# Performance work log

Hardware: AMD Instinct MI355X
Metric: run time of the kernel (lower is better)

The kernel has to match this reference:

```python
import jax, jax.numpy as jnp
import numpy as np

N_VERT = 100000
N_EDGE = 50000
NNZ = 3200000
IN_CH = 256
OUT_CH = 64


def setup_inputs() -> dict:
    key = jax.random.key(0)
    k1, k2, k3, k4, k5, k6 = jax.random.split(key, 6)
    X = jax.random.normal(k1, (N_VERT, IN_CH), dtype=jnp.float32)
    W = jax.random.normal(k2, (OUT_CH, IN_CH), dtype=jnp.float32) * (IN_CH ** -0.5)
    degE = jax.random.uniform(k3, (N_EDGE,), dtype=jnp.float32, minval=0.01, maxval=1.0)
    degV = jax.random.uniform(k4, (N_VERT,), dtype=jnp.float32, minval=0.01, maxval=1.0)
    Wdiag = jnp.ones((N_EDGE,), dtype=jnp.float32)
    v_idx = jax.random.randint(k5, (NNZ,), 0, N_VERT, dtype=jnp.int32)
    e_idx = jax.random.randint(k6, (NNZ,), 0, N_EDGE, dtype=jnp.int32)
    return {"X": X, "W": W, "degE": degE, "degV": degV, "Wdiag": Wdiag,
            "v_idx": v_idx, "e_idx": e_idx}


def reference(X, W, degE, degV, Wdiag, v_idx, e_idx):
    # Dense projection: [N, in] @ [in, out] -> [N, out]
    Xp = jnp.einsum('ni,oi->no', X, W)
    # Stage 1: vertex -> hyperedge aggregation, degE + Wdiag normalization
    Xe = jax.ops.segment_sum(Xp[v_idx], e_idx, num_segments=N_EDGE)
    Xe = Xe * (degE * Wdiag)[:, None]
    # Stage 2: hyperedge -> vertex aggregation, degV normalization
    Xv = jax.ops.segment_sum(Xe[e_idx], v_idx, num_segments=N_VERT)
    Xv = Xv * degV[:, None]
    return Xv
```

## Files before the change

### kernel.cpp

```cpp
#include <hip/hip_runtime.h>

#define NV   100000
#define NE   50000
#define NNZ  3200000
#define KIN  256
#define KOUT 64

#define NB    256
#define CHUNK (NNZ / NB)
#define TS    6250
#define NBE   782
#define NBV   1563
#define NBINS (NBE + NBV)
#define LSCAN (NBINS * NB)
#define NBLK_SCAN ((LSCAN + 1023) / 1024)

#define ECAP_E 6144
#define ECAP_V 4096

typedef short short8 __attribute__((ext_vector_type(8)));
typedef float f32x4  __attribute__((ext_vector_type(4)));

__device__ __forceinline__ unsigned short f2bf(float f) {
    union { float f; unsigned u; } c{f};
    const unsigned lsb = (c.u >> 16) & 1u;
    return (unsigned short)((c.u + 0x7FFFu + lsb) >> 16);
}
__device__ __forceinline__ float bf2f_lo(unsigned u) {
    union { unsigned u; float f; } c{u << 16};
    return c.f;
}
__device__ __forceinline__ float bf2f_hi(unsigned u) {
    union { unsigned u; float f; } c{u & 0xFFFF0000u};
    return c.f;
}
__device__ __forceinline__ short8 pack8(const float4 lo, const float4 hi) {
    short8 r;
    r[0] = (short)f2bf(lo.x); r[1] = (short)f2bf(lo.y);
    r[2] = (short)f2bf(lo.z); r[3] = (short)f2bf(lo.w);
    r[4] = (short)f2bf(hi.x); r[5] = (short)f2bf(hi.y);
    r[6] = (short)f2bf(hi.z); r[7] = (short)f2bf(hi.w);
    return r;
}

__global__ __launch_bounds__(256) void k_wb(const float* __restrict__ W,
                                            unsigned short* __restrict__ Wb) {
    const int i = blockIdx.x * 256 + threadIdx.x;
    Wb[i] = f2bf(W[i]);
}

__global__ __launch_bounds__(256) void k_project(const float* __restrict__ X,
                                                 const unsigned short* __restrict__ Wb,
                                                 unsigned short* __restrict__ Xpb) {
    const int tid  = threadIdx.x;
    const int lane = tid & 63;
    const int wv   = tid >> 6;
    const int l15  = lane & 15;
    const int l4   = lane >> 4;
    const int rbase = blockIdx.x * 128 + wv * 32;

    const int r0 = min(rbase + l15,      NV - 1);
    const int r1 = min(rbase + 16 + l15, NV - 1);
    const float* xp0 = X + (size_t)r0 * KIN + l4 * 8;
    const float* xp1 = X + (size_t)r1 * KIN + l4 * 8;
    const unsigned short* wp = Wb + (size_t)l15 * KIN + l4 * 8;

    f32x4 acc[2][4];
#pragma unroll
    for (int t = 0; t < 2; ++t)
#pragma unroll
        for (int g = 0; g < 4; ++g)
            acc[t][g] = (f32x4){0.f, 0.f, 0.f, 0.f};

#pragma unroll
    for (int s = 0; s < 8; ++s) {
        const int k0 = s * 32;
        const float4 a0lo = *(const float4*)(xp0 + k0);
        const float4 a0hi = *(const float4*)(xp0 + k0 + 4);
        const float4 a1lo = *(const float4*)(xp1 + k0);
        const float4 a1hi = *(const float4*)(xp1 + k0 + 4);
        short8 b[4];
#pragma unroll
        for (int g = 0; g < 4; ++g)
            b[g] = *(const short8*)(wp + (size_t)g * 16 * KIN + k0);
        const short8 a0 = pack8(a0lo, a0hi);
        const short8 a1 = pack8(a1lo, a1hi);
#pragma unroll
        for (int g = 0; g < 4; ++g) {
            acc[0][g] = __builtin_amdgcn_mfma_f32_16x16x32_bf16(a0, b[g], acc[0][g], 0, 0, 0);
            acc[1][g] = __builtin_amdgcn_mfma_f32_16x16x32_bf16(a1, b[g], acc[1][g], 0, 0, 0);
        }
    }

#pragma unroll
    for (int t = 0; t < 2; ++t)
#pragma unroll
        for (int i = 0; i < 4; ++i) {
            const int r = rbase + t * 16 + l4 * 4 + i;
            if (r < NV) {
#pragma unroll
                for (int g = 0; g < 4; ++g)
                    Xpb[(size_t)r * KOUT + g * 16 + l15] = f2bf(acc[t][g][i]);
            }
        }
}

__global__ __launch_bounds__(1024) void k_hist(const int* __restrict__ v_idx,
                                               const int* __restrict__ e_idx,
                                               int* __restrict__ mat) {
    __shared__ int h[NBINS];
    const int b = blockIdx.x, tid = threadIdx.x;
    for (int i = tid; i < NBINS; i += 1024) h[i] = 0;
    __syncthreads();
    const int base = b * CHUNK;
    for (int i = tid; i < CHUNK; i += 1024) {
        atomicAdd(&h[e_idx[base + i] >> 6], 1);
        atomicAdd(&h[NBE + (v_idx[base + i] >> 6)], 1);
    }
    __syncthreads();
    for (int j = tid; j < NBINS; j += 1024) mat[j * NB + b] = h[j];
}

__global__ __launch_bounds__(1024) void k_scan1(int* __restrict__ mat,
                                                int* __restrict__ bsum) {
    __shared__ int buf[1024];
    const int tid = threadIdx.x;
    const int i = blockIdx.x * 1024 + tid;
    const int v = (i < LSCAN) ? mat[i] : 0;
    buf[tid] = v;
    __syncthreads();
    for (int d = 1; d < 1024; d <<= 1) {
        int t = (tid >= d) ? buf[tid - d] : 0;
        __syncthreads();
        buf[tid] += t;
        __syncthreads();
    }
    if (i < LSCAN) mat[i] = buf[tid] - v;
    if (tid == 1023) bsum[blockIdx.x] = buf[1023];
}

__global__ __launch_bounds__(1024) void k_scan2(int* __restrict__ bsum) {
    __shared__ int buf[1024];
    const int tid = threadIdx.x;
    const int v = (tid < NBLK_SCAN) ? bsum[tid] : 0;
    buf[tid] = v;
    __syncthreads();
    for (int d = 1; d < 1024; d <<= 1) {
        int t = (tid >= d) ? buf[tid - d] : 0;
        __syncthreads();
        buf[tid] += t;
        __syncthreads();
    }
    if (tid < NBLK_SCAN) bsum[tid] = buf[tid] - v;
}

__global__ __launch_bounds__(1024) void k_scan3(int* __restrict__ mat,
                                                const int* __restrict__ bsum) {
    const int i = blockIdx.x * 1024 + threadIdx.x;
    if (i < LSCAN) mat[i] += bsum[blockIdx.x];
}

template <int SIDE, int NBIN>
__global__ __launch_bounds__(1024) void k_partsort(const int* __restrict__ v_idx,
                                                   const int* __restrict__ e_idx,
                                                   const int* __restrict__ mat,
                                                   unsigned* __restrict__ part) {
    __shared__ unsigned sbuf[TS];
    __shared__ unsigned short binbuf[TS];
    __shared__ int hist[NBIN], pfx[NBIN], cur[NBIN], gdst[NBIN];
    const int b = blockIdx.x, tid = threadIdx.x;
    const int rowOff = SIDE ? NBE : 0;
    const int sub    = SIDE ? NNZ : 0;

    for (int j = tid; j < NBIN; j += 1024)
        gdst[j] = mat[(rowOff + j) * NB + b] - sub;

    const int base = b * CHUNK;
    for (int tile = 0; tile < CHUNK / TS; ++tile) {
        __syncthreads();
        for (int j = tid; j < NBIN; j += 1024) hist[j] = 0;
        __syncthreads();

        int sb[7]; unsigned svv[7];
#pragma unroll
        for (int s = 0; s < 7; ++s) {
            const int li = s * 1024 + tid;
            sb[s] = -1;
            if (li < TS) {
                const int i = base + tile * TS + li;
                const int v = v_idx[i], e = e_idx[i];
                int bin; unsigned val;
                if (SIDE == 0) { bin = e >> 6; val = (unsigned)v | ((unsigned)(e & 63) << 17); }
                else           { bin = v >> 6; val = (unsigned)e | ((unsigned)(v & 63) << 17); }
                atomicAdd(&hist[bin], 1);
                sb[s] = bin; svv[s] = val;
            }
        }
        __syncthreads();

        if (tid < 64) {
            int carry = 0;
            for (int c = 0; c < NBIN; c += 64) {
                const int j = c + tid;
                const int h = (j < NBIN) ? hist[j] : 0;
                int x = h;
#pragma unroll
                for (int d = 1; d < 64; d <<= 1) {
                    const int y = __shfl_up(x, d, 64);
                    if (tid >= d) x += y;
                }
                if (j < NBIN) pfx[j] = carry + x - h;
                carry += __shfl(x, 63, 64);
            }
        }
        __syncthreads();
        for (int j = tid; j < NBIN; j += 1024) cur[j] = pfx[j];
        __syncthreads();

#pragma unroll
        for (int s = 0; s < 7; ++s) {
            if (sb[s] >= 0) {
                const int p = atomicAdd(&cur[sb[s]], 1);
                sbuf[p] = svv[s];
                binbuf[p] = (unsigned short)sb[s];
            }
        }
        __syncthreads();

        for (int li = tid; li < TS; li += 1024) {
            const int bin = binbuf[li];
            part[gdst[bin] + (li - pfx[bin])] = sbuf[li];
        }
        __syncthreads();
        for (int j = tid; j < NBIN; j += 1024) gdst[j] += cur[j] - pfx[j];
    }
}

__global__ __launch_bounds__(1024) void k_sortgatherE(const unsigned* __restrict__ part,
                                                      const int* __restrict__ mat,
                                                      const unsigned short* __restrict__ Xpb,
                                                      const float* __restrict__ degE,
                                                      const float* __restrict__ Wdiag,
                                                      unsigned short* __restrict__ Xeb) {
    __shared__ unsigned sbuf[ECAP_E];
    __shared__ int hist[64], cur[64], pfx[65];
    const int b = blockIdx.x, tid = threadIdx.x;
    const int base = mat[b * NB];
    const int end  = (b == NBE - 1) ? NNZ : mat[(b + 1) * NB];
    const int nb = end - base;

    if (tid < 64) hist[tid] = 0;
    __syncthreads();
    for (int i = tid; i < nb; i += 1024)
        atomicAdd(&hist[(part[base + i] >> 17) & 63], 1);
    __syncthreads();
    if (tid == 0) {
        int s = 0;
        for (int k = 0; k < 64; ++k) { pfx[k] = s; cur[k] = s; s += hist[k]; }
        pfx[64] = s;
    }
    __syncthreads();
    for (int i = tid; i < nb; i += 1024) {
        const unsigned u = part[base + i];
        const int p = atomicAdd(&cur[(u >> 17) & 63], 1);
        sbuf[p] = u & 0x1FFFFu;
    }
    __syncthreads();

    const int wv = tid >> 6, lane = tid & 63;
    const int q = lane >> 3, sl = lane & 7;
#pragma unroll
    for (int j = 0; j < 4; ++j) {
        const int le = wv * 4 + j;
        const int e_id = (b << 6) + le;
        const int s0 = pfx[le];
        const int n  = pfx[le + 1] - s0;
        float a0 = 0.f, a1 = 0.f, a2 = 0.f, a3 = 0.f,
              a4 = 0.f, a5 = 0.f, a6 = 0.f, a7 = 0.f;
        const int nf = n >> 3;
        int t = 0;
        for (; t + 4 <= nf; t += 4) {
            int idx[4]; uint4 u4[4];
#pragma unroll
            for (int z = 0; z < 4; ++z) idx[z] = (int)sbuf[s0 + 8 * (t + z) + q];
#pragma unroll
            for (int z = 0; z < 4; ++z)
                u4[z] = *(const uint4*)&Xpb[(size_t)idx[z] * KOUT + 8 * sl];
#pragma unroll
            for (int z = 0; z < 4; ++z) {
                a0 += bf2f_lo(u4[z].x); a1 += bf2f_hi(u4[z].x);
                a2 += bf2f_lo(u4[z].y); a3 += bf2f_hi(u4[z].y);
                a4 += bf2f_lo(u4[z].z); a5 += bf2f_hi(u4[z].z);
                a6 += bf2f_lo(u4[z].w); a7 += bf2f_hi(u4[z].w);
            }
        }
        for (; t < nf; ++t) {
            const int idx = (int)sbuf[s0 + 8 * t + q];
            const uint4 u = *(const uint4*)&Xpb[(size_t)idx * KOUT + 8 * sl];
            a0 += bf2f_lo(u.x); a1 += bf2f_hi(u.x);
            a2 += bf2f_lo(u.y); a3 += bf2f_hi(u.y);
            a4 += bf2f_lo(u.z); a5 += bf2f_hi(u.z);
            a6 += bf2f_lo(u.w); a7 += bf2f_hi(u.w);
        }
        if (n & 7) {
            const int src = nf * 8 + q;
            if (src < n) {
                const int idx = (int)sbuf[s0 + src];
                const uint4 u = *(const uint4*)&Xpb[(size_t)idx * KOUT + 8 * sl];
                a0 += bf2f_lo(u.x); a1 += bf2f_hi(u.x);
                a2 += bf2f_lo(u.y); a3 += bf2f_hi(u.y);
                a4 += bf2f_lo(u.z); a5 += bf2f_hi(u.z);
                a6 += bf2f_lo(u.w); a7 += bf2f_hi(u.w);
            }
        }
#pragma unroll
        for (int d = 8; d < 64; d <<= 1) {
            a0 += __shfl_xor(a0, d, 64); a1 += __shfl_xor(a1, d, 64);
            a2 += __shfl_xor(a2, d, 64); a3 += __shfl_xor(a3, d, 64);
            a4 += __shfl_xor(a4, d, 64); a5 += __shfl_xor(a5, d, 64);
            a6 += __shfl_xor(a6, d, 64); a7 += __shfl_xor(a7, d, 64);
        }
        if (q == 0 && e_id < NE) {
            const float s = degE[e_id] * Wdiag[e_id];
            uint4 pk;
            pk.x = (unsigned)f2bf(a0 * s) | ((unsigned)f2bf(a1 * s) << 16);
            pk.y = (unsigned)f2bf(a2 * s) | ((unsigned)f2bf(a3 * s) << 16);
            pk.z = (unsigned)f2bf(a4 * s) | ((unsigned)f2bf(a5 * s) << 16);
            pk.w = (unsigned)f2bf(a6 * s) | ((unsigned)f2bf(a7 * s) << 16);
            *(uint4*)&Xeb[(size_t)e_id * KOUT + 8 * sl] = pk;
        }
    }
}

__global__ __launch_bounds__(1024) void k_sortgatherV(const unsigned* __restrict__ part,
                                                      const int* __restrict__ mat,
                                                      const unsigned short* __restrict__ Xeb,
                                                      const float* __restrict__ degV,
                                                      float* __restrict__ out) {
    __shared__ unsigned sbuf[ECAP_V];
    __shared__ int hist[64], cur[64], pfx[65];
    const int b = blockIdx.x, tid = threadIdx.x;
    const int base = mat[NBE * NB + b * NB] - NNZ;
    const int end  = (b == NBV - 1) ? NNZ : (mat[NBE * NB + (b + 1) * NB] - NNZ);
    const int nb = end - base;

    if (tid < 64) hist[tid] = 0;
    __syncthreads();
    for (int i = tid; i < nb; i += 1024)
        atomicAdd(&hist[(part[base + i] >> 17) & 63], 1);
    __syncthreads();
    if (tid == 0) {
        int s = 0;
        for (int k = 0; k < 64; ++k) { pfx[k] = s; cur[k] = s; s += hist[k]; }
        pfx[64] = s;
    }
    __syncthreads();
    for (int i = tid; i < nb; i += 1024) {
        const unsigned u = part[base + i];
        const int p = atomicAdd(&cur[(u >> 17) & 63], 1);
        sbuf[p] = u & 0x1FFFFu;
    }
    __syncthreads();

    const int wv = tid >> 6, lane = tid & 63;
    const int q = lane >> 3, sl = lane & 7;
#pragma unroll
    for (int j = 0; j < 4; ++j) {
        const int lv = wv * 4 + j;
        const int v_id = (b << 6) + lv;
        const int s0 = pfx[lv];
        const int n  = pfx[lv + 1] - s0;
        float a0 = 0.f, a1 = 0.f, a2 = 0.f, a3 = 0.f,
              a4 = 0.f, a5 = 0.f, a6 = 0.f, a7 = 0.f;
        const int nf = n >> 3;
        int t = 0;
        for (; t + 4 <= nf; t += 4) {
            int idx[4]; uint4 u4[4];
#pragma unroll
            for (int z = 0; z < 4; ++z) idx[z] = (int)sbuf[s0 + 8 * (t + z) + q];
#pragma unroll
            for (int z = 0; z < 4; ++z)
                u4[z] = *(const uint4*)&Xeb[(size_t)idx[z] * KOUT + 8 * sl];
#pragma unroll
            for (int z = 0; z < 4; ++z) {
                a0 += bf2f_lo(u4[z].x); a1 += bf2f_hi(u4[z].x);
                a2 += bf2f_lo(u4[z].y); a3 += bf2f_hi(u4[z].y);
                a4 += bf2f_lo(u4[z].z); a5 += bf2f_hi(u4[z].z);
                a6 += bf2f_lo(u4[z].w); a7 += bf2f_hi(u4[z].w);
            }
        }
        for (; t < nf; ++t) {
            const int idx = (int)sbuf[s0 + 8 * t + q];
            const uint4 u = *(const uint4*)&Xeb[(size_t)idx * KOUT + 8 * sl];
            a0 += bf2f_lo(u.x); a1 += bf2f_hi(u.x);
            a2 += bf2f_lo(u.y); a3 += bf2f_hi(u.y);
            a4 += bf2f_lo(u.z); a5 += bf2f_hi(u.z);
            a6 += bf2f_lo(u.w); a7 += bf2f_hi(u.w);
        }
        if (n & 7) {
            const int src = nf * 8 + q;
            if (src < n) {
                const int idx = (int)sbuf[s0 + src];
                const uint4 u = *(const uint4*)&Xeb[(size_t)idx * KOUT + 8 * sl];
                a0 += bf2f_lo(u.x); a1 += bf2f_hi(u.x);
                a2 += bf2f_lo(u.y); a3 += bf2f_hi(u.y);
                a4 += bf2f_lo(u.z); a5 += bf2f_hi(u.z);
                a6 += bf2f_lo(u.w); a7 += bf2f_hi(u.w);
            }
        }
#pragma unroll
        for (int d = 8; d < 64; d <<= 1) {
            a0 += __shfl_xor(a0, d, 64); a1 += __shfl_xor(a1, d, 64);
            a2 += __shfl_xor(a2, d, 64); a3 += __shfl_xor(a3, d, 64);
            a4 += __shfl_xor(a4, d, 64); a5 += __shfl_xor(a5, d, 64);
            a6 += __shfl_xor(a6, d, 64); a7 += __shfl_xor(a7, d, 64);
        }
        if (q == 0 && v_id < NV) {
            const float s = degV[v_id];
            *(float4*)&out[(size_t)v_id * KOUT + 8 * sl] =
                make_float4(a0 * s, a1 * s, a2 * s, a3 * s);
            *(float4*)&out[(size_t)v_id * KOUT + 8 * sl + 4] =
                make_float4(a4 * s, a5 * s, a6 * s, a7 * s);
        }
    }
}

extern "C" void kernel_launch(void* const* d_in, const int* in_sizes, int n_in,
                              void* d_out, int out_size, void* d_ws, size_t ws_size,
                              hipStream_t stream) {
    const float* X     = (const float*)d_in[0];
    const float* W     = (const float*)d_in[1];
    const float* degE  = (const float*)d_in[2];
    const float* degV  = (const float*)d_in[3];
    const float* Wdiag = (const float*)d_in[4];
    const int*   v_idx = (const int*)d_in[5];
    const int*   e_idx = (const int*)d_in[6];
    float* out = (float*)d_out;

    unsigned short* Xpb  = (unsigned short*)d_ws;
    unsigned short* Xeb  = Xpb + (size_t)NV * KOUT;
    unsigned*       partE = (unsigned*)(Xeb + (size_t)NE * KOUT);
    unsigned*       partV = partE + NNZ;
    int*            mat   = (int*)(partV + NNZ);
    int*            bsum  = mat + LSCAN;
    unsigned short* Wb    = (unsigned short*)(bsum + ((NBLK_SCAN + 3) & ~3));

    k_wb<<<(KIN * KOUT) / 256, 256, 0, stream>>>(W, Wb);
    k_project<<<(NV + 127) / 128, 256, 0, stream>>>(X, Wb, Xpb);

    k_hist<<<NB, 1024, 0, stream>>>(v_idx, e_idx, mat);
    k_scan1<<<NBLK_SCAN, 1024, 0, stream>>>(mat, bsum);
    k_scan2<<<1, 1024, 0, stream>>>(bsum);
    k_scan3<<<NBLK_SCAN, 1024, 0, stream>>>(mat, bsum);

    k_partsort<0, NBE><<<NB, 1024, 0, stream>>>(v_idx, e_idx, mat, partE);
    k_partsort<1, NBV><<<NB, 1024, 0, stream>>>(v_idx, e_idx, mat, partV);

    k_sortgatherE<<<NBE, 1024, 0, stream>>>(partE, mat, Xpb, degE, Wdiag, Xeb);
    k_sortgatherV<<<NBV, 1024, 0, stream>>>(partV, mat, Xeb, degV, out);
}
```

Before: 226.0 us.

## Merge projection with histogram and both partition sorts into single launches

Fuses the dense projection and the index histogram into one launch that splits blocks by role, with 1024-thread projection blocks each covering 512 rows. It also merges the E-side and V-side partition sorts into one launch of 2*NB blocks. The aim is to let independent work overlap on the GPU and to cut launch gaps and tail underutilisation. In exchange, the merged kernels carry the larger shared-memory footprint and register pressure of whichever role needs more, which can lower occupancy.

New measurement: 207.8 us. 8.0% less time.

```diff
diff --git a/kernel.cpp b/kernel.cpp
--- a/kernel.cpp
+++ b/kernel.cpp
@@ -15,6 +15,8 @@
 #define LSCAN (NBINS * NB)
 #define NBLK_SCAN ((LSCAN + 1023) / 1024)
 
+#define PROJ_BLKS 196
+
 #define ECAP_E 6144
 #define ECAP_V 4096
 
@@ -49,76 +51,78 @@
     Wb[i] = f2bf(W[i]);
 }
 
-__global__ __launch_bounds__(256) void k_project(const float* __restrict__ X,
-                                                 const unsigned short* __restrict__ Wb,
-                                                 unsigned short* __restrict__ Xpb) {
-    const int tid  = threadIdx.x;
-    const int lane = tid & 63;
-    const int wv   = tid >> 6;
-    const int l15  = lane & 15;
-    const int l4   = lane >> 4;
-    const int rbase = blockIdx.x * 128 + wv * 32;
-
-    const int r0 = min(rbase + l15,      NV - 1);
-    const int r1 = min(rbase + 16 + l15, NV - 1);
-    const float* xp0 = X + (size_t)r0 * KIN + l4 * 8;
-    const float* xp1 = X + (size_t)r1 * KIN + l4 * 8;
-    const unsigned short* wp = Wb + (size_t)l15 * KIN + l4 * 8;
-
-    f32x4 acc[2][4];
-#pragma unroll
-    for (int t = 0; t < 2; ++t)
-#pragma unroll
-        for (int g = 0; g < 4; ++g)
-            acc[t][g] = (f32x4){0.f, 0.f, 0.f, 0.f};
-
-#pragma unroll
-    for (int s = 0; s < 8; ++s) {
-        const int k0 = s * 32;
-        const float4 a0lo = *(const float4*)(xp0 + k0);
-        const float4 a0hi = *(const float4*)(xp0 + k0 + 4);
-        const float4 a1lo = *(const float4*)(xp1 + k0);
-        const float4 a1hi = *(const float4*)(xp1 + k0 + 4);
-        short8 b[4];
-#pragma unroll
-        for (int g = 0; g < 4; ++g)
-            b[g] = *(const short8*)(wp + (size_t)g * 16 * KIN + k0);
-        const short8 a0 = pack8(a0lo, a0hi);
-        const short8 a1 = pack8(a1lo, a1hi);
-#pragma unroll
-        for (int g = 0; g < 4; ++g) {
-            acc[0][g] = __builtin_amdgcn_mfma_f32_16x16x32_bf16(a0, b[g], acc[0][g], 0, 0, 0);
-            acc[1][g] = __builtin_amdgcn_mfma_f32_16x16x32_bf16(a1, b[g], acc[1][g], 0, 0, 0);
-        }
-    }
-
-#pragma unroll
-    for (int t = 0; t < 2; ++t)
-#pragma unroll
-        for (int i = 0; i < 4; ++i) {
-            const int r = rbase + t * 16 + l4 * 4 + i;
-            if (r < NV) {
-#pragma unroll
-                for (int g = 0; g < 4; ++g)
-                    Xpb[(size_t)r * KOUT + g * 16 + l15] = f2bf(acc[t][g][i]);
-            }
-        }
-}
-
-__global__ __launch_bounds__(1024) void k_hist(const int* __restrict__ v_idx,
-                                               const int* __restrict__ e_idx,
-                                               int* __restrict__ mat) {
+__global__ __launch_bounds__(1024) void k_projhist(const float* __restrict__ X,
+                                                   const unsigned short* __restrict__ Wb,
+                                                   unsigned short* __restrict__ Xpb,
+                                                   const int* __restrict__ v_idx,
+                                                   const int* __restrict__ e_idx,
+                                                   int* __restrict__ mat) {
     __shared__ int h[NBINS];
-    const int b = blockIdx.x, tid = threadIdx.x;
-    for (int i = tid; i < NBINS; i += 1024) h[i] = 0;
-    __syncthreads();
-    const int base = b * CHUNK;
-    for (int i = tid; i < CHUNK; i += 1024) {
-        atomicAdd(&h[e_idx[base + i] >> 6], 1);
-        atomicAdd(&h[NBE + (v_idx[base + i] >> 6)], 1);
-    }
-    __syncthreads();
-    for (int j = tid; j < NBINS; j += 1024) mat[j * NB + b] = h[j];
+    if (blockIdx.x < PROJ_BLKS) {
+        const int tid  = threadIdx.x;
+        const int lane = tid & 63;
+        const int wv   = tid >> 6;
+        const int l15  = lane & 15;
+        const int l4   = lane >> 4;
+        const int rbase = blockIdx.x * 512 + wv * 32;
+
+        const int r0 = min(rbase + l15,      NV - 1);
+        const int r1 = min(rbase + 16 + l15, NV - 1);
+        const float* xp0 = X + (size_t)r0 * KIN + l4 * 8;
+        const float* xp1 = X + (size_t)r1 * KIN + l4 * 8;
+        const unsigned short* wp = Wb + (size_t)l15 * KIN + l4 * 8;
+
+        f32x4 acc[2][4];
+#pragma unroll
+        for (int t = 0; t < 2; ++t)
+#pragma unroll
+            for (int g = 0; g < 4; ++g)
+                acc[t][g] = (f32x4){0.f, 0.f, 0.f, 0.f};
+
+#pragma unroll
+        for (int s = 0; s < 8; ++s) {
+            const int k0 = s * 32;
+            const float4 a0lo = *(const float4*)(xp0 + k0);
+            const float4 a0hi = *(const float4*)(xp0 + k0 + 4);
+            const float4 a1lo = *(const float4*)(xp1 + k0);
+            const float4 a1hi = *(const float4*)(xp1 + k0 + 4);
+            short8 b[4];
+#pragma unroll
+            for (int g = 0; g < 4; ++g)
+                b[g] = *(const short8*)(wp + (size_t)g * 16 * KIN + k0);
+            const short8 a0 = pack8(a0lo, a0hi);
+            const short8 a1 = pack8(a1lo, a1hi);
+#pragma unroll
+            for (int g = 0; g < 4; ++g) {
+                acc[0][g] = __builtin_amdgcn_mfma_f32_16x16x32_bf16(a0, b[g], acc[0][g], 0, 0, 0);
+                acc[1][g] = __builtin_amdgcn_mfma_f32_16x16x32_bf16(a1, b[g], acc[1][g], 0, 0, 0);
+            }
+        }
+
+#pragma unroll
+        for (int t = 0; t < 2; ++t)
+#pragma unroll
+            for (int i = 0; i < 4; ++i) {
+                const int r = rbase + t * 16 + l4 * 4 + i;
+                if (r < NV) {
+#pragma unroll
+                    for (int g = 0; g < 4; ++g)
+                        Xpb[(size_t)r * KOUT + g * 16 + l15] = f2bf(acc[t][g][i]);
+                }
+            }
+    } else {
+        const int bb = blockIdx.x - PROJ_BLKS;
+        const int tid = threadIdx.x;
+        for (int i = tid; i < NBINS; i += 1024) h[i] = 0;
+        __syncthreads();
+        const int base = bb * CHUNK;
+        for (int i = tid; i < CHUNK; i += 1024) {
+            atomicAdd(&h[e_idx[base + i] >> 6], 1);
+            atomicAdd(&h[NBE + (v_idx[base + i] >> 6)], 1);
+        }
+        __syncthreads();
+        for (int j = tid; j < NBINS; j += 1024) mat[j * NB + bb] = h[j];
+    }
 }
 
 __global__ __launch_bounds__(1024) void k_scan1(int* __restrict__ mat,
@@ -160,25 +164,29 @@
     if (i < LSCAN) mat[i] += bsum[blockIdx.x];
 }
 
-template <int SIDE, int NBIN>
-__global__ __launch_bounds__(1024) void k_partsort(const int* __restrict__ v_idx,
-                                                   const int* __restrict__ e_idx,
-                                                   const int* __restrict__ mat,
-                                                   unsigned* __restrict__ part) {
+__global__ __launch_bounds__(1024) void k_partsort2(const int* __restrict__ v_idx,
+                                                    const int* __restrict__ e_idx,
+                                                    const int* __restrict__ mat,
+                                                    unsigned* __restrict__ partE,
+                                                    unsigned* __restrict__ partV) {
     __shared__ unsigned sbuf[TS];
     __shared__ unsigned short binbuf[TS];
-    __shared__ int hist[NBIN], pfx[NBIN], cur[NBIN], gdst[NBIN];
-    const int b = blockIdx.x, tid = threadIdx.x;
-    const int rowOff = SIDE ? NBE : 0;
-    const int sub    = SIDE ? NNZ : 0;
-
-    for (int j = tid; j < NBIN; j += 1024)
+    __shared__ int hist[NBV], pfx[NBV], cur[NBV], gdst[NBV];
+    const int side = (blockIdx.x >= NB) ? 1 : 0;
+    const int b = blockIdx.x - side * NB;
+    const int tid = threadIdx.x;
+    const int nbin = side ? NBV : NBE;
+    const int rowOff = side ? NBE : 0;
+    const int sub    = side ? NNZ : 0;
+    unsigned* __restrict__ part = side ? partV : partE;
+
+    for (int j = tid; j < nbin; j += 1024)
         gdst[j] = mat[(rowOff + j) * NB + b] - sub;
 
     const int base = b * CHUNK;
     for (int tile = 0; tile < CHUNK / TS; ++tile) {
         __syncthreads();
-        for (int j = tid; j < NBIN; j += 1024) hist[j] = 0;
+        for (int j = tid; j < nbin; j += 1024) hist[j] = 0;
         __syncthreads();
 
         int sb[7]; unsigned svv[7];
@@ -190,7 +198,7 @@
                 const int i = base + tile * TS + li;
                 const int v = v_idx[i], e = e_idx[i];
                 int bin; unsigned val;
-                if (SIDE == 0) { bin = e >> 6; val = (unsigned)v | ((unsigned)(e & 63) << 17); }
+                if (side == 0) { bin = e >> 6; val = (unsigned)v | ((unsigned)(e & 63) << 17); }
                 else           { bin = v >> 6; val = (unsigned)e | ((unsigned)(v & 63) << 17); }
                 atomicAdd(&hist[bin], 1);
                 sb[s] = bin; svv[s] = val;
@@ -200,21 +208,21 @@
 
         if (tid < 64) {
             int carry = 0;
-            for (int c = 0; c < NBIN; c += 64) {
+            for (int c = 0; c < nbin; c += 64) {
                 const int j = c + tid;
-                const int h = (j < NBIN) ? hist[j] : 0;
+                const int h = (j < nbin) ? hist[j] : 0;
                 int x = h;
 #pragma unroll
                 for (int d = 1; d < 64; d <<= 1) {
                     const int y = __shfl_up(x, d, 64);
                     if (tid >= d) x += y;
                 }
-                if (j < NBIN) pfx[j] = carry + x - h;
+                if (j < nbin) pfx[j] = carry + x - h;
                 carry += __shfl(x, 63, 64);
             }
         }
         __syncthreads();
-        for (int j = tid; j < NBIN; j += 1024) cur[j] = pfx[j];
+        for (int j = tid; j < nbin; j += 1024) cur[j] = pfx[j];
         __syncthreads();
 
 #pragma unroll
@@ -232,7 +240,7 @@
             part[gdst[bin] + (li - pfx[bin])] = sbuf[li];
         }
         __syncthreads();
-        for (int j = tid; j < NBIN; j += 1024) gdst[j] += cur[j] - pfx[j];
+        for (int j = tid; j < nbin; j += 1024) gdst[j] += cur[j] - pfx[j];
     }
 }
 
@@ -446,15 +454,14 @@
     unsigned short* Wb    = (unsigned short*)(bsum + ((NBLK_SCAN + 3) & ~3));
 
     k_wb<<<(KIN * KOUT) / 256, 256, 0, stream>>>(W, Wb);
-    k_project<<<(NV + 127) / 128, 256, 0, stream>>>(X, Wb, Xpb);
-
-    k_hist<<<NB, 1024, 0, stream>>>(v_idx, e_idx, mat);
+
+    k_projhist<<<PROJ_BLKS + NB, 1024, 0, stream>>>(X, Wb, Xpb, v_idx, e_idx, mat);
+
     k_scan1<<<NBLK_SCAN, 1024, 0, stream>>>(mat, bsum);
     k_scan2<<<1, 1024, 0, stream>>>(bsum);
     k_scan3<<<NBLK_SCAN, 1024, 0, stream>>>(mat, bsum);
 
-    k_partsort<0, NBE><<<NB, 1024, 0, stream>>>(v_idx, e_idx, mat, partE);
-    k_partsort<1, NBV><<<NB, 1024, 0, stream>>>(v_idx, e_idx, mat, partV);
+    k_partsort2<<<2 * NB, 1024, 0, stream>>>(v_idx, e_idx, mat, partE, partV);
 
     k_sortgatherE<<<NBE, 1024, 0, stream>>>(partE, mat, Xpb, degE, Wdiag, Xeb);
     k_sortgatherV<<<NBV, 1024, 0, stream>>>(partV, mat, Xeb, degV, out);
```
